# Performance work log

Measured on AMD Instinct MI355X. Metric: run time of the kernel, lower is better.

The kernel has to match this reference:

```python
import jax, jax.numpy as jnp
import numpy as np

N, D, K, L = 65536, 512, 1024, 4
TEMPERATURE = 1.0


def setup_inputs() -> dict:
    key = jax.random.key(0)
    k1, k2 = jax.random.split(key)
    inputs = jax.random.normal(k1, (N, D), dtype=jnp.float32)
    # L separate (non-shared) codebooks, first n_embed rows of each nn.Embedding
    # (the extra padding row is never selected by argmin, so we omit it).
    codebooks = jax.random.normal(k2, (L, K, D), dtype=jnp.float32) * 0.02
    return {"inputs": inputs, "codebooks": codebooks}


def _quantize_level(residual, cb):
    # addmm-based squared-distance: ||r||^2 + ||c||^2 - 2 r @ c^T, then / temperature
    r_sq = jnp.sum(residual * residual, axis=-1, keepdims=True)        # [N,1]
    c_sq = jnp.sum(cb * cb, axis=-1)[None, :]                          # [1,K]
    dists = (r_sq + c_sq - 2.0 * jnp.einsum('nd,kd->nk', residual, cb)) / TEMPERATURE
    idx = jnp.argmin(dists, axis=-1)                                   # [N]
    embeds = cb[idx]                                                   # [N,D] gather
    return embeds, idx


def reference(inputs, codebooks):
    """Residual quantization: sequentially quantize the residual with each
    level's codebook (eval-mode forward: no EMA buffer updates).
    Returns (quantized, codes) where quantized = sum of per-level embeds."""
    residual = inputs
    quant = jnp.zeros_like(inputs)
    codes = []
    for l in range(codebooks.shape[0]):  # L is small and fixed
        embeds, idx = _quantize_level(residual, codebooks[l])
        quant = quant + embeds
        residual = residual - embeds
        codes.append(idx)
    codes = jnp.stack(codes, axis=-1)  # [N, L] int32
    return quant, codes
```

## Files before the change

kernel.cpp:

```cpp
#include <hip/hip_runtime.h>

#define NROWS_TOTAL 65536
#define DDIM 512
#define KCODES 1024
#define LLEV 4
#define ROWS 32
#define KT 512
#define CODES_OFF ((size_t)NROWS_TOTAL * DDIM)
#define MARGIN 0.0625f

typedef __attribute__((address_space(1))) const unsigned int glb_u32_t;
typedef __attribute__((address_space(3))) unsigned int lds_u32_t;
typedef __attribute__((ext_vector_type(8))) short bf16x8;
typedef __attribute__((ext_vector_type(4))) float f32x4;

__device__ __forceinline__ void gload_lds16(const void* g, void* l) {
  __builtin_amdgcn_global_load_lds((glb_u32_t*)g, (lds_u32_t*)l, 16, 0, 0);
}

__device__ __forceinline__ unsigned short f2bf(float f) {
  union { float f; unsigned u; } c; c.f = f;
  return (unsigned short)((c.u + 0x7fffu + ((c.u >> 16) & 1u)) >> 16);
}
__device__ __forceinline__ float bf2f(short h) {
  union { unsigned u; float f; } c; c.u = ((unsigned)(unsigned short)h) << 16;
  return c.f;
}
__device__ __forceinline__ bf16x8 packbf8(float4 a, float4 b) {
  bf16x8 r;
  r[0] = (short)f2bf(a.x); r[1] = (short)f2bf(a.y);
  r[2] = (short)f2bf(a.z); r[3] = (short)f2bf(a.w);
  r[4] = (short)f2bf(b.x); r[5] = (short)f2bf(b.y);
  r[6] = (short)f2bf(b.z); r[7] = (short)f2bf(b.w);
  return r;
}

__global__ void csq_kernel(const float* __restrict__ cb, float* __restrict__ csq) {
  int row  = blockIdx.x * 4 + (threadIdx.x >> 6);
  int lane = threadIdx.x & 63;
  const float* p = cb + (size_t)row * DDIM;
  float s = 0.f;
#pragma unroll
  for (int i = 0; i < 8; ++i) { float v = p[lane + 64 * i]; s = fmaf(v, v, s); }
#pragma unroll
  for (int off = 32; off > 0; off >>= 1) s += __shfl_down(s, off, 64);
  if (lane == 0) csq[row] = s;
}

__global__ void pack_kernel(const float* __restrict__ cb, unsigned short* __restrict__ cbB) {
  const int gid = blockIdx.x * 256 + threadIdx.x;
  const int g = gid & 3, ks = (gid >> 2) & 15, c = (gid >> 6) & 1023, l = gid >> 16;
  const float* p = cb + ((size_t)(l * KCODES + c)) * DDIM + ks * 32 + g * 8;
  float4 v0 = *(const float4*)p, v1 = *(const float4*)(p + 4);
  bf16x8 r = packbf8(v0, v1);
  *(bf16x8*)(cbB + ((((size_t)(l * 16 + ks) * 64 + (c >> 4)) * 4 + g) * 16 + (c & 15)) * 8) = r;
}

__launch_bounds__(512, 4)
__global__ void rq_mfma(const float* __restrict__ x, const float* __restrict__ cb,
                        const float* __restrict__ csq,
                        const unsigned short* __restrict__ cbB,
                        float* __restrict__ out) {
  __shared__ __align__(16) unsigned short ls_b[2][2][4096];
  __shared__ __align__(16) float ls_csq[1024];
  __shared__ unsigned long long ls_flags[128][16];
  __shared__ int ls_mi[128];
  __shared__ int ls_cnt[128];
  __shared__ int ls_hist[LLEV][128];

  const int tid = threadIdx.x;
  const int w = tid >> 6, lane = tid & 63;
  const int g = lane >> 4, c15 = lane & 15;
  const int rowbase = blockIdx.x * 128;
  const int arow_g = rowbase + w * 16 + c15;

  bf16x8 areg[16];
#pragma unroll
  for (int ks = 0; ks < 16; ++ks) {
    const float* p = x + (size_t)arow_g * DDIM + ks * 32 + g * 8;
    float4 v0 = *(const float4*)p, v1 = *(const float4*)(p + 4);
    areg[ks] = packbf8(v0, v1);
  }

  auto issue_pair = [&](int lvl, int p, int buf) {
    const int t = 2 * p + (w >> 2);
    const unsigned short* src = cbB + (size_t)lvl * 524288 + (size_t)(t & 15) * 32768
                                + (size_t)(t >> 4) * 4096 + (w & 3) * 1024 + lane * 8;
    unsigned short* dst = &ls_b[buf][w >> 2][(w & 3) * 1024 + lane * 8];
    gload_lds16(src, dst);
    gload_lds16(src + 512, dst + 512);
  };

  for (int l = 0; l < LLEV; ++l) {
    if (tid < 256) *(float4*)&ls_csq[tid * 4] = *(const float4*)(csq + l * KCODES + tid * 4);

    float mv[4]; int mi[4]; unsigned long long flg[4];
#pragma unroll
    for (int i = 0; i < 4; ++i) { mv[i] = 3.4e38f; mi[i] = 0; flg[i] = 0ull; }

    if (l == 0) issue_pair(0, 0, 0);

    f32x4 acc[8];
    for (int u = 0; u < 64; ++u) {
      const int cg = u >> 3, kk = u & 7;
      const int buf = u & 1;

      __syncthreads();

      if (u < 63) issue_pair(l, u + 1, buf ^ 1);
      else if (l < LLEV - 1) issue_pair(l + 1, 0, buf ^ 1);

      if (kk == 0) {
#pragma unroll
        for (int f = 0; f < 8; ++f) acc[f] = (f32x4){0.f, 0.f, 0.f, 0.f};
      }

      const unsigned short* cb0 = &ls_b[buf][0][g * 128 + c15 * 8];
      const unsigned short* cb1 = &ls_b[buf][1][g * 128 + c15 * 8];
#pragma unroll
      for (int f = 0; f < 8; ++f) {
        bf16x8 bB0 = *(const bf16x8*)(cb0 + f * 512);
        acc[f] = __builtin_amdgcn_mfma_f32_16x16x32_bf16(areg[2 * kk], bB0, acc[f], 0, 0, 0);
        bf16x8 bB1 = *(const bf16x8*)(cb1 + f * 512);
        acc[f] = __builtin_amdgcn_mfma_f32_16x16x32_bf16(areg[2 * kk + 1], bB1, acc[f], 0, 0, 0);
      }

      if (kk == 7) {
        float qv[8][4];
#pragma unroll
        for (int f = 0; f < 8; ++f) {
          float cs = ls_csq[cg * 128 + f * 16 + c15];
#pragma unroll
          for (int i = 0; i < 4; ++i) qv[f][i] = fmaf(-2.0f, acc[f][i], cs);
        }
#pragma unroll
        for (int i = 0; i < 4; ++i) {
          float lv = qv[0][i]; int li = cg * 128 + c15;
#pragma unroll
          for (int f = 1; f < 8; ++f) {
            int code = cg * 128 + f * 16 + c15;
            if (qv[f][i] < lv) { lv = qv[f][i]; li = code; }
          }
#pragma unroll
          for (int off = 1; off < 16; off <<= 1) {
            float ov = __shfl_xor(lv, off, 64);
            int oi = __shfl_xor(li, off, 64);
            if (ov < lv || (ov == lv && oi < li)) { lv = ov; li = oi; }
          }
          if (lv < mv[i] || (lv == mv[i] && li < mi[i])) { mv[i] = lv; mi[i] = li; }
          float thr = mv[i] + MARGIN;
#pragma unroll
          for (int f = 0; f < 8; ++f)
            if (qv[f][i] <= thr) flg[i] |= (1ull << (cg * 8 + f));
        }
      }
    }

    const int row0 = w * 16 + g * 4;
#pragma unroll
    for (int i = 0; i < 4; ++i) {
      int cnt = __popcll(flg[i]);
#pragma unroll
      for (int off = 1; off < 16; off <<= 1) cnt += __shfl_xor(cnt, off, 64);
      ls_flags[row0 + i][c15] = flg[i];
      if (c15 == 0) { ls_mi[row0 + i] = mi[i]; ls_cnt[row0 + i] = cnt; }
    }

    for (int r = 0; r < 16; ++r) {
      const int row = w * 16 + r;
      if (ls_cnt[row] > 1) {
        const int grow = rowbase + row;
        const float* xp = x + (size_t)grow * DDIM + lane * 8;
        float4 a0 = *(const float4*)xp;
        float4 a1 = *(const float4*)(xp + 4);
        float rs0 = a0.x, rs1 = a0.y, rs2 = a0.z, rs3 = a0.w;
        float rs4 = a1.x, rs5 = a1.y, rs6 = a1.z, rs7 = a1.w;
        for (int lp = 0; lp < l; ++lp) {
          const float* cp = cb + ((size_t)(lp * KCODES + ls_hist[lp][row])) * DDIM + lane * 8;
          float4 e0 = *(const float4*)cp;
          float4 e1 = *(const float4*)(cp + 4);
          rs0 -= e0.x; rs1 -= e0.y; rs2 -= e0.z; rs3 -= e0.w;
          rs4 -= e1.x; rs5 -= e1.y; rs6 -= e1.z; rs7 -= e1.w;
        }
        float pr = 0.f;
        pr = fmaf(rs0, rs0, pr); pr = fmaf(rs1, rs1, pr);
        pr = fmaf(rs2, rs2, pr); pr = fmaf(rs3, rs3, pr);
        pr = fmaf(rs4, rs4, pr); pr = fmaf(rs5, rs5, pr);
        pr = fmaf(rs6, rs6, pr); pr = fmaf(rs7, rs7, pr);
#pragma unroll
        for (int off = 1; off < 64; off <<= 1) pr += __shfl_xor(pr, off, 64);
        float bs = 3.4e38f; int bc = 0x7fffffff;
        for (int j16 = 0; j16 < 16; ++j16) {
          unsigned long long b = ls_flags[row][j16];
          while (b) {
            int bit = __builtin_ctzll(b); b &= b - 1;
            int code = ((bit >> 3) << 7) + ((bit & 7) << 4) + j16;
            const float* cp = cb + ((size_t)(l * KCODES + code)) * DDIM + lane * 8;
            float4 e0 = *(const float4*)cp;
            float4 e1 = *(const float4*)(cp + 4);
            float pd = 0.f;
            pd = fmaf(rs0, e0.x, pd); pd = fmaf(rs1, e0.y, pd);
            pd = fmaf(rs2, e0.z, pd); pd = fmaf(rs3, e0.w, pd);
            pd = fmaf(rs4, e1.x, pd); pd = fmaf(rs5, e1.y, pd);
            pd = fmaf(rs6, e1.z, pd); pd = fmaf(rs7, e1.w, pd);
#pragma unroll
            for (int off = 1; off < 64; off <<= 1) pd += __shfl_xor(pd, off, 64);
            float s = (pr + ls_csq[code]) - 2.0f * pd;
            if (s < bs || (s == bs && code < bc)) { bs = s; bc = code; }
          }
        }
        if (lane == 0) ls_mi[row] = bc;
      }
    }
    __syncthreads();

    if (tid < 128) ls_hist[l][tid] = ls_mi[tid];
    if (l < LLEV - 1) {
      const int idxr = ls_mi[w * 16 + c15];
      const float* crow = cb + ((size_t)(l * KCODES + idxr)) * DDIM;
#pragma unroll
      for (int ks = 0; ks < 16; ++ks) {
        const float* p = crow + ks * 32 + g * 8;
        float4 v0 = *(const float4*)p, v1 = *(const float4*)(p + 4);
        bf16x8 a = areg[ks];
        float4 n0, n1;
        n0.x = bf2f(a[0]) - v0.x; n0.y = bf2f(a[1]) - v0.y;
        n0.z = bf2f(a[2]) - v0.z; n0.w = bf2f(a[3]) - v0.w;
        n1.x = bf2f(a[4]) - v1.x; n1.y = bf2f(a[5]) - v1.y;
        n1.z = bf2f(a[6]) - v1.z; n1.w = bf2f(a[7]) - v1.w;
        areg[ks] = packbf8(n0, n1);
      }
    }
  }

  __syncthreads();
  if (tid < 128) {
    float4 cv = make_float4((float)ls_hist[0][tid], (float)ls_hist[1][tid],
                            (float)ls_hist[2][tid], (float)ls_hist[3][tid]);
    *(float4*)(out + CODES_OFF + (size_t)(rowbase + tid) * LLEV) = cv;
  }
  {
    const int row = tid >> 2;
    const int d0 = (tid & 3) * 128;
    const float* p0 = cb + ((size_t)(0 * KCODES + ls_hist[0][row])) * DDIM + d0;
    const float* p1 = cb + ((size_t)(1 * KCODES + ls_hist[1][row])) * DDIM + d0;
    const float* p2 = cb + ((size_t)(2 * KCODES + ls_hist[2][row])) * DDIM + d0;
    const float* p3 = cb + ((size_t)(3 * KCODES + ls_hist[3][row])) * DDIM + d0;
    float* op = out + (size_t)(rowbase + row) * DDIM + d0;
#pragma unroll 8
    for (int ch = 0; ch < 32; ++ch) {
      float4 e0 = *(const float4*)(p0 + ch * 4);
      float4 e1 = *(const float4*)(p1 + ch * 4);
      float4 e2 = *(const float4*)(p2 + ch * 4);
      float4 e3 = *(const float4*)(p3 + ch * 4);
      float4 q;
      q.x = ((e0.x + e1.x) + e2.x) + e3.x;
      q.y = ((e0.y + e1.y) + e2.y) + e3.y;
      q.z = ((e0.z + e1.z) + e2.z) + e3.z;
      q.w = ((e0.w + e1.w) + e2.w) + e3.w;
      *(float4*)(op + ch * 4) = q;
    }
  }
}

#define DC 16
#define RSTRIDE 20

__launch_bounds__(256, 2)
__global__ void rq_kernel(const float* __restrict__ x, const float* __restrict__ cb,
                          const float* __restrict__ csq, float* __restrict__ out) {
  __shared__ float ls_cbT[DC * KT];
  __shared__ float ls_r[ROWS * RSTRIDE];
  __shared__ float ls_minv[ROWS * 64];
  __shared__ int   ls_mini[ROWS * 64];
  __shared__ float ls_rsqp[ROWS * 8];
  __shared__ float ls_rsq[ROWS];
  __shared__ int   ls_idx[ROWS];

  const int tid = threadIdx.x;
  const int rg  = tid >> 6;
  const int kg  = tid & 63;
  const int own_row = tid >> 3;
  const int own_d0  = (tid & 7) * 64;
  const int rowbase = blockIdx.x * ROWS;

  float rres[64];
  {
    const float4* xp = (const float4*)(x + (size_t)(rowbase + own_row) * DDIM + own_d0);
#pragma unroll
    for (int i = 0; i < 16; ++i) {
      float4 v = xp[i];
      rres[4*i] = v.x; rres[4*i+1] = v.y; rres[4*i+2] = v.z; rres[4*i+3] = v.w;
    }
  }

  for (int l = 0; l < LLEV; ++l) {
    {
      float p = 0.f;
#pragma unroll
      for (int i = 0; i < 64; ++i) p = fmaf(rres[i], rres[i], p);
      ls_rsqp[own_row * 8 + (tid & 7)] = p;
    }
    __syncthreads();
    if (tid < ROWS) {
      float s = 0.f;
#pragma unroll
      for (int i = 0; i < 8; ++i) s += ls_rsqp[tid * 8 + i];
      ls_rsq[tid] = s;
    }

    float mv[8]; int mi[8];
#pragma unroll
    for (int r = 0; r < 8; ++r) { mv[r] = 3.4e38f; mi[r] = 0; }

    const float* cbl = cb + (size_t)l * KCODES * DDIM;

    for (int kt = 0; kt < KCODES / KT; ++kt) {
      float acc[8][8];
#pragma unroll
      for (int r = 0; r < 8; ++r)
#pragma unroll
        for (int c = 0; c < 8; ++c) acc[r][c] = 0.f;

      for (int dc = 0; dc < DDIM / DC; ++dc) {
        __syncthreads();
        {
          int krow = tid >> 2;
          int dcol = (tid & 3) * 4;
#pragma unroll
          for (int p = 0; p < 8; ++p) {
            int klocal = p * 64 + krow;
            float4 v = *(const float4*)(cbl + (size_t)(kt * KT + klocal) * DDIM + dc * DC + dcol);
            ls_cbT[(dcol + 0) * KT + klocal] = v.x;
            ls_cbT[(dcol + 1) * KT + klocal] = v.y;
            ls_cbT[(dcol + 2) * KT + klocal] = v.z;
            ls_cbT[(dcol + 3) * KT + klocal] = v.w;
          }
        }
        if ((tid & 7) == (dc >> 2)) {
          switch (dc & 3) {
            case 0:
#pragma unroll
              for (int i = 0; i < 4; ++i)
                *(float4*)&ls_r[own_row * RSTRIDE + i * 4] =
                  make_float4(rres[0*16+4*i], rres[0*16+4*i+1], rres[0*16+4*i+2], rres[0*16+4*i+3]);
              break;
            case 1:
#pragma unroll
              for (int i = 0; i < 4; ++i)
                *(float4*)&ls_r[own_row * RSTRIDE + i * 4] =
                  make_float4(rres[1*16+4*i], rres[1*16+4*i+1], rres[1*16+4*i+2], rres[1*16+4*i+3]);
              break;
            case 2:
#pragma unroll
              for (int i = 0; i < 4; ++i)
                *(float4*)&ls_r[own_row * RSTRIDE + i * 4] =
                  make_float4(rres[2*16+4*i], rres[2*16+4*i+1], rres[2*16+4*i+2], rres[2*16+4*i+3]);
              break;
            default:
#pragma unroll
              for (int i = 0; i < 4; ++i)
                *(float4*)&ls_r[own_row * RSTRIDE + i * 4] =
                  make_float4(rres[3*16+4*i], rres[3*16+4*i+1], rres[3*16+4*i+2], rres[3*16+4*i+3]);
              break;
          }
        }
        __syncthreads();
        for (int ds4 = 0; ds4 < DC / 4; ++ds4) {
          float rvf[4][8];
#pragma unroll
          for (int r = 0; r < 8; ++r) {
            float4 t = *(const float4*)&ls_r[(rg * 8 + r) * RSTRIDE + ds4 * 4];
            rvf[0][r] = t.x; rvf[1][r] = t.y; rvf[2][r] = t.z; rvf[3][r] = t.w;
          }
#pragma unroll
          for (int jj = 0; jj < 4; ++jj) {
            float4 cv0 = *(const float4*)&ls_cbT[(ds4 * 4 + jj) * KT + 4 * kg];
            float4 cv1 = *(const float4*)&ls_cbT[(ds4 * 4 + jj) * KT + KT / 2 + 4 * kg];
#pragma unroll
            for (int r = 0; r < 8; ++r) {
              float rv = rvf[jj][r];
              acc[r][0] = fmaf(rv, cv0.x, acc[r][0]);
              acc[r][1] = fmaf(rv, cv0.y, acc[r][1]);
              acc[r][2] = fmaf(rv, cv0.z, acc[r][2]);
              acc[r][3] = fmaf(rv, cv0.w, acc[r][3]);
              acc[r][4] = fmaf(rv, cv1.x, acc[r][4]);
              acc[r][5] = fmaf(rv, cv1.y, acc[r][5]);
              acc[r][6] = fmaf(rv, cv1.z, acc[r][6]);
              acc[r][7] = fmaf(rv, cv1.w, acc[r][7]);
            }
          }
        }
      }
#pragma unroll
      for (int g = 0; g < 2; ++g)
#pragma unroll
        for (int c = 0; c < 4; ++c) {
          int k = kt * KT + g * (KT / 2) + 4 * kg + c;
          float cs = csq[l * KCODES + k];
#pragma unroll
          for (int r = 0; r < 8; ++r) {
            float s = (ls_rsq[rg * 8 + r] + cs) - 2.0f * acc[r][g * 4 + c];
            if (s < mv[r]) { mv[r] = s; mi[r] = k; }
          }
        }
    }

#pragma unroll
    for (int r = 0; r < 8; ++r) {
      ls_minv[(rg * 8 + r) * 64 + kg] = mv[r];
      ls_mini[(rg * 8 + r) * 64 + kg] = mi[r];
    }
    __syncthreads();
    if (tid < ROWS) {
      float bv = ls_minv[tid * 64]; int bi = ls_mini[tid * 64];
      for (int i = 1; i < 64; ++i) {
        float v = ls_minv[tid * 64 + i]; int ii = ls_mini[tid * 64 + i];
        if (v < bv || (v == bv && ii < bi)) { bv = v; bi = ii; }
      }
      ls_idx[tid] = bi;
      out[CODES_OFF + (size_t)(rowbase + tid) * LLEV + l] = (float)bi;
    }
    __syncthreads();
    {
      int idx = ls_idx[own_row];
      const float4* cp = (const float4*)(cbl + (size_t)idx * DDIM + own_d0);
#pragma unroll
      for (int i = 0; i < 16; ++i) {
        float4 v = cp[i];
        rres[4*i]   -= v.x; rres[4*i+1] -= v.y;
        rres[4*i+2] -= v.z; rres[4*i+3] -= v.w;
      }
    }
  }

  {
    const float4* xp = (const float4*)(x + (size_t)(rowbase + own_row) * DDIM + own_d0);
    float4* op = (float4*)(out + (size_t)(rowbase + own_row) * DDIM + own_d0);
#pragma unroll
    for (int i = 0; i < 16; ++i) {
      float4 v = xp[i];
      op[i] = make_float4(v.x - rres[4*i],   v.y - rres[4*i+1],
                          v.z - rres[4*i+2], v.w - rres[4*i+3]);
    }
  }
}

extern "C" void kernel_launch(void* const* d_in, const int* in_sizes, int n_in,
                              void* d_out, int out_size, void* d_ws, size_t ws_size,
                              hipStream_t stream) {
  const float* x  = (const float*)d_in[0];
  const float* cb = (const float*)d_in[1];
  float* out = (float*)d_out;
  float* csq = (float*)d_ws;
  unsigned short* cbB = (unsigned short*)((float*)d_ws + 4096);

  const size_t need = 4096 * sizeof(float)
                    + (size_t)LLEV * 16 * 64 * 4 * 16 * 8 * sizeof(unsigned short);

  csq_kernel<<<dim3((LLEV * KCODES) / 4), dim3(256), 0, stream>>>(cb, csq);
  if (ws_size >= need) {
    pack_kernel<<<dim3(1024), dim3(256), 0, stream>>>(cb, cbB);
    rq_mfma<<<dim3(NROWS_TOTAL / 128), dim3(512), 0, stream>>>(x, cb, csq, cbB, out);
  } else {
    rq_kernel<<<dim3(NROWS_TOTAL / ROWS), dim3(256), 0, stream>>>(x, cb, csq, out);
  }
}
```

Before: 1.391 ms.

## Process two 16-row A tiles per wave to reuse each codebook B fragment

Each wave now holds two 16-row A tiles in registers and issues two MFMAs per loaded B fragment, doubling rows per block to 256 and halving the grid. The aim is to halve the LDS codebook reads and global-to-LDS codebook traffic per row, raising MFMA density per barrier. The cost is roughly doubled register use for A tiles and accumulators, so launch bounds drop to 2 blocks per SM, which lowers occupancy and latency hiding. The 256-block grid may also leave part of the GPU idle or unevenly loaded.

```diff
diff --git a/kernel.cpp b/kernel.cpp
--- a/kernel.cpp
+++ b/kernel.cpp
@@ -56,30 +56,60 @@
   *(bf16x8*)(cbB + ((((size_t)(l * 16 + ks) * 64 + (c >> 4)) * 4 + g) * 16 + (c & 15)) * 8) = r;
 }
 
-__launch_bounds__(512, 4)
+#define EPI(ACC, MV, MI, FLG)                                                   \
+  {                                                                             \
+    float qv[8][4];                                                             \
+    _Pragma("unroll") for (int f = 0; f < 8; ++f) {                             \
+      float cs = ls_csq[cg * 128 + f * 16 + c15];                               \
+      _Pragma("unroll") for (int i = 0; i < 4; ++i)                             \
+        qv[f][i] = fmaf(-2.0f, ACC[f][i], cs);                                  \
+    }                                                                           \
+    _Pragma("unroll") for (int i = 0; i < 4; ++i) {                             \
+      float lv = qv[0][i]; int li = cg * 128 + c15;                             \
+      _Pragma("unroll") for (int f = 1; f < 8; ++f) {                           \
+        int code = cg * 128 + f * 16 + c15;                                     \
+        if (qv[f][i] < lv) { lv = qv[f][i]; li = code; }                        \
+      }                                                                         \
+      _Pragma("unroll") for (int off = 1; off < 16; off <<= 1) {                \
+        float ov = __shfl_xor(lv, off, 64);                                     \
+        int oi = __shfl_xor(li, off, 64);                                       \
+        if (ov < lv || (ov == lv && oi < li)) { lv = ov; li = oi; }             \
+      }                                                                         \
+      if (lv < MV[i] || (lv == MV[i] && li < MI[i])) { MV[i] = lv; MI[i] = li; }\
+      float thr = MV[i] + MARGIN;                                               \
+      _Pragma("unroll") for (int f = 0; f < 8; ++f)                             \
+        if (qv[f][i] <= thr) FLG[i] |= (1ull << (cg * 8 + f));                  \
+    }                                                                           \
+  }
+
+__launch_bounds__(512, 2)
 __global__ void rq_mfma(const float* __restrict__ x, const float* __restrict__ cb,
                         const float* __restrict__ csq,
                         const unsigned short* __restrict__ cbB,
                         float* __restrict__ out) {
   __shared__ __align__(16) unsigned short ls_b[2][2][4096];
   __shared__ __align__(16) float ls_csq[1024];
-  __shared__ unsigned long long ls_flags[128][16];
-  __shared__ int ls_mi[128];
-  __shared__ int ls_cnt[128];
-  __shared__ int ls_hist[LLEV][128];
+  __shared__ unsigned long long ls_flags[256][16];
+  __shared__ int ls_mi[256];
+  __shared__ int ls_cnt[256];
+  __shared__ int ls_hist[LLEV][256];
 
   const int tid = threadIdx.x;
   const int w = tid >> 6, lane = tid & 63;
   const int g = lane >> 4, c15 = lane & 15;
-  const int rowbase = blockIdx.x * 128;
-  const int arow_g = rowbase + w * 16 + c15;
-
-  bf16x8 areg[16];
+  const int rowbase = blockIdx.x * 256;
+  const int arow0 = rowbase + w * 32 + c15;
+  const int arow1 = arow0 + 16;
+
+  bf16x8 areg0[16], areg1[16];
 #pragma unroll
   for (int ks = 0; ks < 16; ++ks) {
-    const float* p = x + (size_t)arow_g * DDIM + ks * 32 + g * 8;
-    float4 v0 = *(const float4*)p, v1 = *(const float4*)(p + 4);
-    areg[ks] = packbf8(v0, v1);
+    const float* p0 = x + (size_t)arow0 * DDIM + ks * 32 + g * 8;
+    float4 a0 = *(const float4*)p0, a1 = *(const float4*)(p0 + 4);
+    areg0[ks] = packbf8(a0, a1);
+    const float* p1 = x + (size_t)arow1 * DDIM + ks * 32 + g * 8;
+    float4 b0 = *(const float4*)p1, b1 = *(const float4*)(p1 + 4);
+    areg1[ks] = packbf8(b0, b1);
   }
 
   auto issue_pair = [&](int lvl, int p, int buf) {
@@ -94,13 +124,17 @@
   for (int l = 0; l < LLEV; ++l) {
     if (tid < 256) *(float4*)&ls_csq[tid * 4] = *(const float4*)(csq + l * KCODES + tid * 4);
 
-    float mv[4]; int mi[4]; unsigned long long flg[4];
-#pragma unroll
-    for (int i = 0; i < 4; ++i) { mv[i] = 3.4e38f; mi[i] = 0; flg[i] = 0ull; }
+    float mv0[4], mv1[4]; int mi0[4], mi1[4];
+    unsigned long long flg0[4], flg1[4];
+#pragma unroll
+    for (int i = 0; i < 4; ++i) {
+      mv0[i] = 3.4e38f; mi0[i] = 0; flg0[i] = 0ull;
+      mv1[i] = 3.4e38f; mi1[i] = 0; flg1[i] = 0ull;
+    }
 
     if (l == 0) issue_pair(0, 0, 0);
 
-    f32x4 acc[8];
+    f32x4 acc0[8], acc1[8];
     for (int u = 0; u < 64; ++u) {
       const int cg = u >> 3, kk = u & 7;
       const int buf = u & 1;
@@ -112,7 +146,10 @@
 
       if (kk == 0) {
 #pragma unroll
-        for (int f = 0; f < 8; ++f) acc[f] = (f32x4){0.f, 0.f, 0.f, 0.f};
+        for (int f = 0; f < 8; ++f) {
+          acc0[f] = (f32x4){0.f, 0.f, 0.f, 0.f};
+          acc1[f] = (f32x4){0.f, 0.f, 0.f, 0.f};
+        }
       }
 
       const unsigned short* cb0 = &ls_b[buf][0][g * 128 + c15 * 8];
@@ -120,54 +157,42 @@
 #pragma unroll
       for (int f = 0; f < 8; ++f) {
         bf16x8 bB0 = *(const bf16x8*)(cb0 + f * 512);
-        acc[f] = __builtin_amdgcn_mfma_f32_16x16x32_bf16(areg[2 * kk], bB0, acc[f], 0, 0, 0);
+        acc0[f] = __builtin_amdgcn_mfma_f32_16x16x32_bf16(areg0[2 * kk], bB0, acc0[f], 0, 0, 0);
+        acc1[f] = __builtin_amdgcn_mfma_f32_16x16x32_bf16(areg1[2 * kk], bB0, acc1[f], 0, 0, 0);
         bf16x8 bB1 = *(const bf16x8*)(cb1 + f * 512);
-        acc[f] = __builtin_amdgcn_mfma_f32_16x16x32_bf16(areg[2 * kk + 1], bB1, acc[f], 0, 0, 0);
+        acc0[f] = __builtin_amdgcn_mfma_f32_16x16x32_bf16(areg0[2 * kk + 1], bB1, acc0[f], 0, 0, 0);
+        acc1[f] = __builtin_amdgcn_mfma_f32_16x16x32_bf16(areg1[2 * kk + 1], bB1, acc1[f], 0, 0, 0);
       }
 
       if (kk == 7) {
-        float qv[8][4];
-#pragma unroll
-        for (int f = 0; f < 8; ++f) {
-          float cs = ls_csq[cg * 128 + f * 16 + c15];
-#pragma unroll
-          for (int i = 0; i < 4; ++i) qv[f][i] = fmaf(-2.0f, acc[f][i], cs);
-        }
-#pragma unroll
-        for (int i = 0; i < 4; ++i) {
-          float lv = qv[0][i]; int li = cg * 128 + c15;
-#pragma unroll
-          for (int f = 1; f < 8; ++f) {
-            int code = cg * 128 + f * 16 + c15;
-            if (qv[f][i] < lv) { lv = qv[f][i]; li = code; }
-          }
-#pragma unroll
-          for (int off = 1; off < 16; off <<= 1) {
-            float ov = __shfl_xor(lv, off, 64);
-            int oi = __shfl_xor(li, off, 64);
-            if (ov < lv || (ov == lv && oi < li)) { lv = ov; li = oi; }
-          }
-          if (lv < mv[i] || (lv == mv[i] && li < mi[i])) { mv[i] = lv; mi[i] = li; }
-          float thr = mv[i] + MARGIN;
-#pragma unroll
-          for (int f = 0; f < 8; ++f)
-            if (qv[f][i] <= thr) flg[i] |= (1ull << (cg * 8 + f));
-        }
-      }
-    }
-
-    const int row0 = w * 16 + g * 4;
-#pragma unroll
-    for (int i = 0; i < 4; ++i) {
-      int cnt = __popcll(flg[i]);
-#pragma unroll
-      for (int off = 1; off < 16; off <<= 1) cnt += __shfl_xor(cnt, off, 64);
-      ls_flags[row0 + i][c15] = flg[i];
-      if (c15 == 0) { ls_mi[row0 + i] = mi[i]; ls_cnt[row0 + i] = cnt; }
-    }
-
-    for (int r = 0; r < 16; ++r) {
-      const int row = w * 16 + r;
+        EPI(acc0, mv0, mi0, flg0)
+        EPI(acc1, mv1, mi1, flg1)
+      }
+    }
+
+    {
+      const int r0 = w * 32 + g * 4;
+#pragma unroll
+      for (int i = 0; i < 4; ++i) {
+        int cnt = __popcll(flg0[i]);
+#pragma unroll
+        for (int off = 1; off < 16; off <<= 1) cnt += __shfl_xor(cnt, off, 64);
+        ls_flags[r0 + i][c15] = flg0[i];
+        if (c15 == 0) { ls_mi[r0 + i] = mi0[i]; ls_cnt[r0 + i] = cnt; }
+      }
+      const int r1 = w * 32 + 16 + g * 4;
+#pragma unroll
+      for (int i = 0; i < 4; ++i) {
+        int cnt = __popcll(flg1[i]);
+#pragma unroll
+        for (int off = 1; off < 16; off <<= 1) cnt += __shfl_xor(cnt, off, 64);
+        ls_flags[r1 + i][c15] = flg1[i];
+        if (c15 == 0) { ls_mi[r1 + i] = mi1[i]; ls_cnt[r1 + i] = cnt; }
+      }
+    }
+
+    for (int r = 0; r < 32; ++r) {
+      const int row = w * 32 + r;
       if (ls_cnt[row] > 1) {
         const int grow = rowbase + row;
         const float* xp = x + (size_t)grow * DDIM + lane * 8;
@@ -214,41 +239,56 @@
     }
     __syncthreads();
 
-    if (tid < 128) ls_hist[l][tid] = ls_mi[tid];
+    if (tid < 256) ls_hist[l][tid] = ls_mi[tid];
     if (l < LLEV - 1) {
-      const int idxr = ls_mi[w * 16 + c15];
-      const float* crow = cb + ((size_t)(l * KCODES + idxr)) * DDIM;
+      const int idx0 = ls_mi[w * 32 + c15];
+      const int idx1 = ls_mi[w * 32 + 16 + c15];
+      const float* cr0 = cb + ((size_t)(l * KCODES + idx0)) * DDIM;
+      const float* cr1 = cb + ((size_t)(l * KCODES + idx1)) * DDIM;
 #pragma unroll
       for (int ks = 0; ks < 16; ++ks) {
-        const float* p = crow + ks * 32 + g * 8;
-        float4 v0 = *(const float4*)p, v1 = *(const float4*)(p + 4);
-        bf16x8 a = areg[ks];
-        float4 n0, n1;
-        n0.x = bf2f(a[0]) - v0.x; n0.y = bf2f(a[1]) - v0.y;
-        n0.z = bf2f(a[2]) - v0.z; n0.w = bf2f(a[3]) - v0.w;
-        n1.x = bf2f(a[4]) - v1.x; n1.y = bf2f(a[5]) - v1.y;
-        n1.z = bf2f(a[6]) - v1.z; n1.w = bf2f(a[7]) - v1.w;
-        areg[ks] = packbf8(n0, n1);
+        {
+          const float* p = cr0 + ks * 32 + g * 8;
+          float4 v0 = *(const float4*)p, v1 = *(const float4*)(p + 4);
+          bf16x8 a = areg0[ks];
+          float4 n0, n1;
+          n0.x = bf2f(a[0]) - v0.x; n0.y = bf2f(a[1]) - v0.y;
+          n0.z = bf2f(a[2]) - v0.z; n0.w = bf2f(a[3]) - v0.w;
+          n1.x = bf2f(a[4]) - v1.x; n1.y = bf2f(a[5]) - v1.y;
+          n1.z = bf2f(a[6]) - v1.z; n1.w = bf2f(a[7]) - v1.w;
+          areg0[ks] = packbf8(n0, n1);
+        }
+        {
+          const float* p = cr1 + ks * 32 + g * 8;
+          float4 v0 = *(const float4*)p, v1 = *(const float4*)(p + 4);
+          bf16x8 a = areg1[ks];
+          float4 n0, n1;
+          n0.x = bf2f(a[0]) - v0.x; n0.y = bf2f(a[1]) - v0.y;
+          n0.z = bf2f(a[2]) - v0.z; n0.w = bf2f(a[3]) - v0.w;
+          n1.x = bf2f(a[4]) - v1.x; n1.y = bf2f(a[5]) - v1.y;
+          n1.z = bf2f(a[6]) - v1.z; n1.w = bf2f(a[7]) - v1.w;
+          areg1[ks] = packbf8(n0, n1);
+        }
       }
     }
   }
 
   __syncthreads();
-  if (tid < 128) {
+  if (tid < 256) {
     float4 cv = make_float4((float)ls_hist[0][tid], (float)ls_hist[1][tid],
                             (float)ls_hist[2][tid], (float)ls_hist[3][tid]);
     *(float4*)(out + CODES_OFF + (size_t)(rowbase + tid) * LLEV) = cv;
   }
   {
-    const int row = tid >> 2;
-    const int d0 = (tid & 3) * 128;
+    const int row = tid >> 1;
+    const int d0 = (tid & 1) * 256;
     const float* p0 = cb + ((size_t)(0 * KCODES + ls_hist[0][row])) * DDIM + d0;
     const float* p1 = cb + ((size_t)(1 * KCODES + ls_hist[1][row])) * DDIM + d0;
     const float* p2 = cb + ((size_t)(2 * KCODES + ls_hist[2][row])) * DDIM + d0;
     const float* p3 = cb + ((size_t)(3 * KCODES + ls_hist[3][row])) * DDIM + d0;
     float* op = out + (size_t)(rowbase + row) * DDIM + d0;
 #pragma unroll 8
-    for (int ch = 0; ch < 32; ++ch) {
+    for (int ch = 0; ch < 64; ++ch) {
       float4 e0 = *(const float4*)(p0 + ch * 4);
       float4 e1 = *(const float4*)(p1 + ch * 4);
       float4 e2 = *(const float4*)(p2 + ch * 4);
@@ -461,7 +501,7 @@
   csq_kernel<<<dim3((LLEV * KCODES) / 4), dim3(256), 0, stream>>>(cb, csq);
   if (ws_size >= need) {
     pack_kernel<<<dim3(1024), dim3(256), 0, stream>>>(cb, cbB);
-    rq_mfma<<<dim3(NROWS_TOTAL / 128), dim3(512), 0, stream>>>(x, cb, csq, cbB, out);
+    rq_mfma<<<dim3(NROWS_TOTAL / 256), dim3(512), 0, stream>>>(x, cb, csq, cbB, out);
   } else {
     rq_kernel<<<dim3(NROWS_TOTAL / ROWS), dim3(256), 0, stream>>>(x, cb, csq, out);
   }
```

Result: slower. 1.712 ms (+23.1%).
